# Optimization experiments

Measured on AMD Instinct MI355X. Metric: run time of the kernel, lower is better.

Reference implementation:

```python
import jax, jax.numpy as jnp
import numpy as np

K = 3          # kernel size
STRIDE = 1
PAD = 1
DIL = 1
K2 = K * K     # number of sampling locations per output pixel


def conv2d(x, w, b, stride=STRIDE, pad=PAD, dil=DIL):
    # x: [B,C,H,W], w: [O,I,K,K], b: [O]
    out = jax.lax.conv_general_dilated(
        x, w, window_strides=(stride, stride),
        padding=[(pad, pad), (pad, pad)], rhs_dilation=(dil, dil),
        dimension_numbers=('NCHW', 'OIHW', 'NCHW'))
    return out + b[None, :, None, None]


def bilinear_sample(x, sy, sx):
    # x: [B,C,H,W]; sy, sx: [B,K2,Ho,Wo] float sampling coords (y, x)
    # zero padding outside the image (torchvision deform_conv2d semantics)
    B, C, H, W = x.shape
    x_flat = x.reshape(B, C, H * W)

    y0 = jnp.floor(sy)
    x0 = jnp.floor(sx)
    wy1 = sy - y0  # frac weights
    wx1 = sx - x0
    wy0 = 1.0 - wy1
    wx0 = 1.0 - wx1

    def gather(yi, xi):
        valid = ((yi >= 0) & (yi < H) & (xi >= 0) & (xi < W)).astype(x.dtype)
        yc = jnp.clip(yi, 0, H - 1).astype(jnp.int32)
        xc = jnp.clip(xi, 0, W - 1).astype(jnp.int32)
        idx = (yc * W + xc).reshape(B, 1, -1)  # [B,1,K2*Ho*Wo]
        v = jnp.take_along_axis(x_flat, idx, axis=2)  # [B,C,K2*Ho*Wo]
        v = v.reshape(B, C, *yi.shape[1:])            # [B,C,K2,Ho,Wo]
        return v * valid[:, None]

    out = (gather(y0,     x0    ) * (wy0 * wx0)[:, None]
         + gather(y0,     x0 + 1) * (wy0 * wx1)[:, None]
         + gather(y0 + 1, x0    ) * (wy1 * wx0)[:, None]
         + gather(y0 + 1, x0 + 1) * (wy1 * wx1)[:, None])
    return out  # [B,C,K2,Ho,Wo]


def setup_inputs() -> dict:
    key = jax.random.key(0)
    ks = jax.random.split(key, 6)
    B, C, H, W = 4, 64, 128, 128
    Cout = 64
    x = jax.random.normal(ks[0], (B, C, H, W), jnp.float32)
    # offset conv: 2*K2 output channels; small init -> small offsets (realistic)
    w_off = jax.random.normal(ks[1], (2 * K2, C, K, K), jnp.float32) * 0.01
    b_off = jnp.zeros((2 * K2,), jnp.float32)
    # mask conv: K2 output channels, sigmoid activation
    w_mask = jax.random.normal(ks[2], (K2, C, K, K), jnp.float32) * 0.01
    b_mask = jnp.zeros((K2,), jnp.float32)  # mask_init_bias = 0
    # main deformable conv weights
    w = jax.random.normal(ks[3], (Cout, C, K, K), jnp.float32) * (1.0 / np.sqrt(C * K2))
    b = jnp.zeros((Cout,), jnp.float32)
    return {"x": x, "w_off": w_off, "b_off": b_off,
            "w_mask": w_mask, "b_mask": b_mask, "w": w, "b": b}


def reference(x, w_off, b_off, w_mask, b_mask, w, b):
    B, C, H, W = x.shape
    Cout = w.shape[0]

    offset = conv2d(x, w_off, b_off)                    # [B,2*K2,Ho,Wo]
    mask = jax.nn.sigmoid(conv2d(x, w_mask, b_mask))    # [B,K2,Ho,Wo]
    Ho, Wo = offset.shape[2], offset.shape[3]

    off = offset.reshape(B, K2, 2, Ho, Wo)
    dy, dx = off[:, :, 0], off[:, :, 1]                 # torchvision layout: (y,x) pairs

    ki = (jnp.arange(K2) // K).astype(jnp.float32)      # kernel row index
    kj = (jnp.arange(K2) % K).astype(jnp.float32)       # kernel col index
    base_y = (jnp.arange(Ho, dtype=jnp.float32) * STRIDE - PAD)[None, :, None] \
             + (ki * DIL)[:, None, None]                # [K2,Ho,1]
    base_x = (jnp.arange(Wo, dtype=jnp.float32) * STRIDE - PAD)[None, None, :] \
             + (kj * DIL)[:, None, None]                # [K2,1,Wo]

    sy = base_y[None] + dy                              # [B,K2,Ho,Wo]
    sx = base_x[None] + dx

    sampled = bilinear_sample(x, sy, sx) * mask[:, None]  # [B,C,K2,Ho,Wo]
    out = jnp.einsum('bckhw,ock->bohw', sampled, w.reshape(Cout, C, K2))
    return out + b[None, :, None, None]
```

## Files before the change

kernel.cpp:

```cpp
#include <hip/hip_runtime.h>
#include <math.h>

typedef __attribute__((ext_vector_type(8))) short short8;
typedef __attribute__((ext_vector_type(4))) float f32x4;
typedef unsigned short ushort_t;
typedef unsigned int uint_t;

#define HH 128
#define WW 128
#define CC 64
#define HWp 16384

__device__ inline ushort_t f2bf(float f) {
    uint_t u = __float_as_uint(f);
    uint_t r = (u + 0x7FFFu + ((u >> 16) & 1u)) >> 16;
    return (ushort_t)r;
}
__device__ inline float blo(uint_t u) { return __uint_as_float(u << 16); }
__device__ inline float bhi(uint_t u) { return __uint_as_float(u & 0xFFFF0000u); }
__device__ inline short8 bc8(uint4 v) { return __builtin_bit_cast(short8, v); }

__device__ inline uint_t pk2(f32x4 wv, uint_t a, uint_t b, uint_t c, uint_t d) {
    float lo = wv.x * blo(a) + wv.y * blo(b) + wv.z * blo(c) + wv.w * blo(d);
    float hi = wv.x * bhi(a) + wv.y * bhi(b) + wv.z * bhi(c) + wv.w * bhi(d);
    uint_t r;
    asm("v_cvt_pk_bf16_f32 %0, %1, %2" : "=v"(r) : "v"(lo), "v"(hi));
    return r;
}
__device__ inline short8 bilerp8(f32x4 wv, uint4 A, uint4 B, uint4 C, uint4 D) {
    uint4 r;
    r.x = pk2(wv, A.x, B.x, C.x, D.x);
    r.y = pk2(wv, A.y, B.y, C.y, D.y);
    r.z = pk2(wv, A.z, B.z, C.z, D.z);
    r.w = pk2(wv, A.w, B.w, C.w, D.w);
    return __builtin_bit_cast(short8, r);
}

__global__ __launch_bounds__(256) void k_prep(const float* __restrict__ x,
        ushort_t* __restrict__ xtb,
        const float* __restrict__ w_off, const float* __restrict__ w_mask,
        const float* __restrict__ w,
        ushort_t* __restrict__ wpom, ushort_t* __restrict__ wpm) {
    __shared__ __align__(16) float tile[64][68];
    int bid = blockIdx.x;
    int t = threadIdx.x;
    if (bid < 1024) {
        int xs = (bid & 1) * 64;
        int y  = (bid >> 1) & 127;
        int b  = bid >> 8;
#pragma unroll
        for (int i = 0; i < 4; ++i) {
            int c  = i * 16 + (t >> 4);
            int xl = (t & 15) << 2;
            float4 v = *(const float4*)&x[(((size_t)b * CC + c) * HH + y) * WW + xs + xl];
            *(float4*)&tile[c][xl] = v;
        }
        __syncthreads();
#pragma unroll
        for (int i = 0; i < 8; ++i) {
            int pxl = i * 8 + (t >> 5);
            int cp  = t & 31;
            float v0 = tile[cp * 2][pxl], v1 = tile[cp * 2 + 1][pxl];
            uint_t pk;
            asm("v_cvt_pk_bf16_f32 %0, %1, %2" : "=v"(pk) : "v"(v0), "v"(v1));
            *(uint_t*)&xtb[(((size_t)b * HH + y) * WW + xs + pxl) * CC + cp * 2] = pk;
        }
    } else {
        int idx = (bid - 1024) * 256 + t;
        if (idx < 18432) {
            int e = idx;
            int j = e & 7, l = (e >> 3) & 63, mf = (e >> 9) & 1, ks = e >> 10;
            int ch = mf * 16 + (l & 15);
            int k = ks * 32 + ((l >> 4) << 3) + j;
            int c = k & 63, kk = k >> 6;
            float v = 0.f;
            if (ch < 18) v = w_off[(ch * CC + c) * 9 + kk];
            else if (ch < 27) v = w_mask[((ch - 18) * CC + c) * 9 + kk];
            wpom[idx] = f2bf(v);
        } else if (idx < 18432 + 36864) {
            int e = idx - 18432;
            int j = e & 7, l = (e >> 3) & 63, mf = (e >> 9) & 3, ks = e >> 11;
            int o = mf * 16 + (l & 15);
            int k = ks * 32 + ((l >> 4) << 3) + j;
            int c = k & 63, kk = k >> 6;
            wpm[e] = f2bf(w[(o * CC + c) * 9 + kk]);
        }
    }
}

__global__ __launch_bounds__(256, 8) void k_conv_om(const ushort_t* __restrict__ xtb,
        const uint4* __restrict__ wpom, const float* __restrict__ b_off,
        const float* __restrict__ b_mask, float* __restrict__ om) {
    __shared__ ushort_t xrow[3 * 34 * 64];
    int blk = blockIdx.x;
    int b = blk >> 9, rem = blk & 511;
    int y = rem >> 2, xw = rem & 3;
    int xbase = (xw << 5) - 1;
    int t = threadIdx.x;

#pragma unroll
    for (int i = 0; i < 4; ++i) {
        int t2 = i * 256 + t;
        if (t2 < 816) {
            int ky = t2 / 272;
            int r2 = t2 - ky * 272;
            int cl = r2 >> 3, cj = r2 & 7;
            int yy = y + ky - 1;
            int xc = xbase + cl;
            bool ok = (yy >= 0) && (yy < HH) && (xc >= 0) && (xc < WW);
            uint4 v = make_uint4(0u, 0u, 0u, 0u);
            if (ok) v = *(const uint4*)&xtb[((size_t)b * HWp + yy * WW + xc) * CC + cj * 8];
            int idx = ((ky * 34 + cl) * 64 + cj * 8) ^ ((cl & 7) << 3);
            *(uint4*)&xrow[idx] = v;
        }
    }
    __syncthreads();

    int lane = t & 63, w = t >> 6;
    int mfc = w & 1, nfc = w >> 1;
    int lm = lane & 15, lg = lane >> 4;
    int pxl = (nfc << 4) + lm;
    f32x4 acc = {};
#pragma unroll
    for (int ks = 0; ks < 18; ++ks) {
        int kk = ks >> 1;
        int kyy = kk / 3, kxx = kk % 3;
        int c0 = (ks & 1) * 32 + lg * 8;
        short8 af = bc8(wpom[(ks * 2 + mfc) * 64 + lane]);
        int cl = pxl + kxx;
        int idx = ((kyy * 34 + cl) * 64 + c0) ^ ((cl & 7) << 3);
        short8 bf = *(const short8*)&xrow[idx];
        acc = __builtin_amdgcn_mfma_f32_16x16x32_bf16(af, bf, acc, 0, 0, 0);
    }
    int xg = (xw << 1) + nfc;
    size_t tb = ((size_t)((b * 128 + y) * 8 + xg)) * 432;
#pragma unroll
    for (int r = 0; r < 4; ++r) {
        int ch = (mfc << 4) + (lg << 2) + r;
        if (ch < 27) {
            float v = acc[r] + (ch < 18 ? b_off[ch] : b_mask[ch - 18]);
            if (ch >= 18) v = 1.f / (1.f + __expf(-v));
            om[tb + ch * 16 + lm] = v;
        }
    }
}

__global__ __launch_bounds__(256, 8) void k_fused(const ushort_t* __restrict__ xtb,
        const float* __restrict__ omt, const uint4* __restrict__ wpm,
        const float* __restrict__ bias, float* __restrict__ out) {
    __shared__ __align__(16) ushort_t sm[16 * 576];
    int blk = blockIdx.x;
    int b = blk >> 10, rem = blk & 1023;
    int y = rem >> 3, xg = rem & 7, xs = xg << 4;
    int t = threadIdx.x, lane = t & 63, w = t >> 6;
    const char* xbB = (const char*)xtb + ((size_t)b << 21);
    const float* omb = omt + ((size_t)((b * 128 + y) * 8 + xg)) * 432;

    float pw0 = 0.f, pw1 = 0.f, pw2 = 0.f, pw3 = 0.f;
    int paT = 0, paB = 0, ppk = 0;
    if (lane < 36) {
        int pxl = lane / 9, k = lane - pxl * 9;
        int px_t = (w << 2) + pxl;
        int ki = k / 3, kj = k - ki * 3;
        int x = xs + px_t;
        float dy = omb[32 * k + px_t];
        float dx = omb[32 * k + 16 + px_t];
        float m  = omb[288 + 16 * k + px_t];
        float sy = (float)(y - 1 + ki) + dy;
        float sx = (float)(x - 1 + kj) + dx;
        float fy = floorf(sy), fx = floorf(sx);
        float wy1 = sy - fy, wx1 = sx - fx;
        float wy0 = 1.f - wy1, wx0 = 1.f - wx1;
        int iy0 = (int)fy, ix0 = (int)fx;
        int iy1 = iy0 + 1, ix1 = ix0 + 1;
        bool vy0 = (iy0 >= 0) & (iy0 < HH);
        bool vy1 = (iy1 >= 0) & (iy1 < HH);
        float wyr0 = vy0 ? wy0 : (vy1 ? wy1 : 0.f);
        int   ry0  = vy0 ? iy0 : (vy1 ? iy1 : 0);
        float wyr1 = (vy0 & vy1) ? wy1 : 0.f;
        int   ry1  = min(max(iy1, 0), HH - 1);
        int bx = min(max(ix0, 0), WW - 2);
        float wxh0 = (bx == ix0) ? wx0 : ((bx == ix1) ? wx1 : 0.f);
        float wxh1 = (bx + 1 == ix1) ? wx1 : ((bx + 1 == ix0) ? wx0 : 0.f);
        pw0 = m * wyr0 * wxh0;
        pw1 = m * wyr0 * wxh1;
        pw2 = m * wyr1 * wxh0;
        pw3 = m * wyr1 * wxh1;
        paT = (int)((uint_t)(((ry0 << 7) + bx) << 7));
        paB = (int)((uint_t)(((ry1 << 7) + bx) << 7));
        ppk = (int)((uint_t)(px_t * 576 + k * 64) |
                    ((uint_t)(((px_t ^ k) & 7) << 3) << 16));
    }

    {
        int g = lane >> 3, j = lane & 7;
        uint_t j16 = (uint_t)(j << 4);
        uint_t jw  = (uint_t)(j << 3);
        int slA = g;
        float wA0 = __shfl(pw0, slA), wA1 = __shfl(pw1, slA);
        float wA2 = __shfl(pw2, slA), wA3 = __shfl(pw3, slA);
        uint_t aTA = (uint_t)__shfl(paT, slA) + j16;
        uint_t aBA = (uint_t)__shfl(paB, slA) + j16;
        uint_t pkA = (uint_t)__shfl(ppk, slA);
        uint4 tlA = *(const uint4*)(xbB + aTA);
        uint4 trA = *(const uint4*)(xbB + aTA + 128);
        uint4 blA = *(const uint4*)(xbB + aBA);
        uint4 brA = *(const uint4*)(xbB + aBA + 128);
#pragma unroll
        for (int r = 0; r < 5; ++r) {
            float wB0, wB1, wB2, wB3;
            uint_t pkB = 0;
            uint4 tlB, trB, blB, brB;
            if (r < 4) {
                int slB = g + (r + 1) * 8; slB = slB > 35 ? 35 : slB;
                wB0 = __shfl(pw0, slB); wB1 = __shfl(pw1, slB);
                wB2 = __shfl(pw2, slB); wB3 = __shfl(pw3, slB);
                uint_t aTB = (uint_t)__shfl(paT, slB) + j16;
                uint_t aBB = (uint_t)__shfl(paB, slB) + j16;
                pkB = (uint_t)__shfl(ppk, slB);
                tlB = *(const uint4*)(xbB + aTB);
                trB = *(const uint4*)(xbB + aTB + 128);
                blB = *(const uint4*)(xbB + aBB);
                brB = *(const uint4*)(xbB + aBB + 128);
            }
            f32x4 wv = { wA0, wA1, wA2, wA3 };
            short8 bf = bilerp8(wv, tlA, trA, blA, brA);
            if (r < 4 || g < 4) {
                uint_t widx = ((pkA & 0xFFFFu) + jw) ^ (pkA >> 16);
                *(short8*)&sm[widx] = bf;
            }
            wA0 = wB0; wA1 = wB1; wA2 = wB2; wA3 = wB3;
            pkA = pkB;
            tlA = tlB; trA = trB; blA = blB; brA = brB;
        }
    }
    __syncthreads();

    int lm = lane & 15, lg = lane >> 4;
    f32x4 acc = {};
#pragma unroll
    for (int ks = 0; ks < 18; ++ks) {
        short8 af = bc8(wpm[((ks << 2) + w) * 64 + lane]);
        int bidx = (lm * 576 + (ks << 5) + (lg << 3)) ^ (((lm ^ (ks >> 1)) & 7) << 3);
        short8 bf = *(const short8*)&sm[bidx];
        acc = __builtin_amdgcn_mfma_f32_16x16x32_bf16(af, bf, acc, 0, 0, 0);
    }
#pragma unroll
    for (int r = 0; r < 4; ++r) {
        int o = (w << 4) + (lg << 2) + r;
        out[(((size_t)b * 64 + o) << 14) + (y << 7) + xs + lm] = acc[r] + bias[o];
    }
}

extern "C" void kernel_launch(void* const* d_in, const int* in_sizes, int n_in,
                              void* d_out, int out_size, void* d_ws, size_t ws_size,
                              hipStream_t stream) {
    const float* x      = (const float*)d_in[0];
    const float* w_off  = (const float*)d_in[1];
    const float* b_off  = (const float*)d_in[2];
    const float* w_mask = (const float*)d_in[3];
    const float* b_mask = (const float*)d_in[4];
    const float* w      = (const float*)d_in[5];
    const float* bias   = (const float*)d_in[6];
    float* out = (float*)d_out;

    char* ws = (char*)d_ws;
    ushort_t* xtb  = (ushort_t*)(ws);
    float*    om   = (float*)(ws + 8388608);
    ushort_t* wpom = (ushort_t*)(ws + 15466496);
    ushort_t* wpm  = (ushort_t*)(ws + 15503360);

    hipLaunchKernelGGL(k_prep, dim3(1240), dim3(256), 0, stream,
                       x, xtb, w_off, w_mask, w, wpom, wpm);
    hipLaunchKernelGGL(k_conv_om, dim3(2048), dim3(256), 0, stream,
                       xtb, (const uint4*)wpom, b_off, b_mask, om);
    hipLaunchKernelGGL(k_fused, dim3(4096), dim3(256), 0, stream,
                       xtb, om, (const uint4*)wpm, bias, out);
}
```

Measured before the change: 48.58 us.

## Precompute bilinear sampling params in offset conv kernel, stream them to fused kernel

The offset/mask conv kernel now stages its outputs in shared memory and computes per-(pixel, tap) bilinear weights, clamped corner addresses and LDS store indices. It writes these as 32-byte records to global memory. The fused kernel loads the precomputed records directly instead of recomputing coordinates and broadcasting them with shuffles, and its occupancy hint drops from 8 to 7. The intermediate buffer grows from 27 floats per pixel to 72 floats per pixel, which increases global write and read traffic between the two kernels.

```diff
diff --git a/kernel.cpp b/kernel.cpp
--- a/kernel.cpp
+++ b/kernel.cpp
@@ -90,8 +90,9 @@
 
 __global__ __launch_bounds__(256, 8) void k_conv_om(const ushort_t* __restrict__ xtb,
         const uint4* __restrict__ wpom, const float* __restrict__ b_off,
-        const float* __restrict__ b_mask, float* __restrict__ om) {
+        const float* __restrict__ b_mask, float* __restrict__ prm) {
     __shared__ ushort_t xrow[3 * 34 * 64];
+    __shared__ float om_t[32][28];
     int blk = blockIdx.x;
     int b = blk >> 9, rem = blk & 511;
     int y = rem >> 2, xw = rem & 3;
@@ -116,37 +117,80 @@
     }
     __syncthreads();
 
-    int lane = t & 63, w = t >> 6;
-    int mfc = w & 1, nfc = w >> 1;
-    int lm = lane & 15, lg = lane >> 4;
-    int pxl = (nfc << 4) + lm;
-    f32x4 acc = {};
-#pragma unroll
-    for (int ks = 0; ks < 18; ++ks) {
-        int kk = ks >> 1;
-        int kyy = kk / 3, kxx = kk % 3;
-        int c0 = (ks & 1) * 32 + lg * 8;
-        short8 af = bc8(wpom[(ks * 2 + mfc) * 64 + lane]);
-        int cl = pxl + kxx;
-        int idx = ((kyy * 34 + cl) * 64 + c0) ^ ((cl & 7) << 3);
-        short8 bf = *(const short8*)&xrow[idx];
-        acc = __builtin_amdgcn_mfma_f32_16x16x32_bf16(af, bf, acc, 0, 0, 0);
-    }
-    int xg = (xw << 1) + nfc;
-    size_t tb = ((size_t)((b * 128 + y) * 8 + xg)) * 432;
-#pragma unroll
-    for (int r = 0; r < 4; ++r) {
-        int ch = (mfc << 4) + (lg << 2) + r;
-        if (ch < 27) {
-            float v = acc[r] + (ch < 18 ? b_off[ch] : b_mask[ch - 18]);
-            if (ch >= 18) v = 1.f / (1.f + __expf(-v));
-            om[tb + ch * 16 + lm] = v;
-        }
-    }
-}
-
-__global__ __launch_bounds__(256, 8) void k_fused(const ushort_t* __restrict__ xtb,
-        const float* __restrict__ omt, const uint4* __restrict__ wpm,
+    {
+        int lane = t & 63, w = t >> 6;
+        int mfc = w & 1, nfc = w >> 1;
+        int lm = lane & 15, lg = lane >> 4;
+        int pxl = (nfc << 4) + lm;
+        f32x4 acc = {};
+#pragma unroll
+        for (int ks = 0; ks < 18; ++ks) {
+            int kk = ks >> 1;
+            int kyy = kk / 3, kxx = kk % 3;
+            int c0 = (ks & 1) * 32 + lg * 8;
+            short8 af = bc8(wpom[(ks * 2 + mfc) * 64 + lane]);
+            int cl = pxl + kxx;
+            int idx = ((kyy * 34 + cl) * 64 + c0) ^ ((cl & 7) << 3);
+            short8 bf = *(const short8*)&xrow[idx];
+            acc = __builtin_amdgcn_mfma_f32_16x16x32_bf16(af, bf, acc, 0, 0, 0);
+        }
+#pragma unroll
+        for (int r = 0; r < 4; ++r) {
+            int ch = (mfc << 4) + (lg << 2) + r;
+            if (ch < 27) {
+                float v = acc[r] + (ch < 18 ? b_off[ch] : b_mask[ch - 18]);
+                if (ch >= 18) v = 1.f / (1.f + __expf(-v));
+                om_t[pxl][ch] = v;
+            }
+        }
+    }
+    __syncthreads();
+
+    size_t tbase = ((size_t)((b * 128 + y) * 8 + (xw << 1))) * 1152;
+#pragma unroll
+    for (int rep = 0; rep < 2; ++rep) {
+        int S = rep * 256 + t;
+        if (S < 288) {
+            int px32 = S / 9, k = S - px32 * 9;
+            int ki = k / 3, kj = k - ki * 3;
+            int x = (xw << 5) + px32;
+            int px_t = px32 & 15;
+            float dy = om_t[px32][2 * k];
+            float dx = om_t[px32][2 * k + 1];
+            float m  = om_t[px32][18 + k];
+            float sy = (float)(y - 1 + ki) + dy;
+            float sx = (float)(x - 1 + kj) + dx;
+            float fy = floorf(sy), fx = floorf(sx);
+            float wy1 = sy - fy, wx1 = sx - fx;
+            float wy0 = 1.f - wy1, wx0 = 1.f - wx1;
+            int iy0 = (int)fy, ix0 = (int)fx;
+            int iy1 = iy0 + 1, ix1 = ix0 + 1;
+            bool vy0 = (iy0 >= 0) & (iy0 < HH);
+            bool vy1 = (iy1 >= 0) & (iy1 < HH);
+            float wyr0 = vy0 ? wy0 : (vy1 ? wy1 : 0.f);
+            int   ry0  = vy0 ? iy0 : (vy1 ? iy1 : 0);
+            float wyr1 = (vy0 & vy1) ? wy1 : 0.f;
+            int   ry1  = min(max(iy1, 0), HH - 1);
+            int bx = min(max(ix0, 0), WW - 2);
+            float wxh0 = (bx == ix0) ? wx0 : ((bx == ix1) ? wx1 : 0.f);
+            float wxh1 = (bx + 1 == ix1) ? wx1 : ((bx + 1 == ix0) ? wx0 : 0.f);
+            f32x4 wv = { m * wyr0 * wxh0, m * wyr0 * wxh1,
+                         m * wyr1 * wxh0, m * wyr1 * wxh1 };
+            f32x4 aux;
+            aux.x = __uint_as_float((uint_t)(((ry0 << 7) + bx) << 7));
+            aux.y = __uint_as_float((uint_t)(((ry1 << 7) + bx) << 7));
+            aux.z = __uint_as_float((uint_t)(px_t * 576 + k * 64) |
+                                    ((uint_t)(((px_t ^ k) & 7) << 3) << 16));
+            aux.w = 0.f;
+            float* pp = prm + tbase + (size_t)S * 8;
+            *(f32x4*)pp = wv;
+            *(f32x4*)(pp + 4) = aux;
+        }
+    }
+}
+
+__global__ __launch_bounds__(256, 7) void k_fused(const ushort_t* __restrict__ xtb,
+        const float* __restrict__ prm, const uint4* __restrict__ wpm,
         const float* __restrict__ bias, float* __restrict__ out) {
     __shared__ __align__(16) ushort_t sm[16 * 576];
     int blk = blockIdx.x;
@@ -154,83 +198,41 @@
     int y = rem >> 3, xg = rem & 7, xs = xg << 4;
     int t = threadIdx.x, lane = t & 63, w = t >> 6;
     const char* xbB = (const char*)xtb + ((size_t)b << 21);
-    const float* omb = omt + ((size_t)((b * 128 + y) * 8 + xg)) * 432;
-
-    float pw0 = 0.f, pw1 = 0.f, pw2 = 0.f, pw3 = 0.f;
-    int paT = 0, paB = 0, ppk = 0;
-    if (lane < 36) {
-        int pxl = lane / 9, k = lane - pxl * 9;
-        int px_t = (w << 2) + pxl;
-        int ki = k / 3, kj = k - ki * 3;
-        int x = xs + px_t;
-        float dy = omb[32 * k + px_t];
-        float dx = omb[32 * k + 16 + px_t];
-        float m  = omb[288 + 16 * k + px_t];
-        float sy = (float)(y - 1 + ki) + dy;
-        float sx = (float)(x - 1 + kj) + dx;
-        float fy = floorf(sy), fx = floorf(sx);
-        float wy1 = sy - fy, wx1 = sx - fx;
-        float wy0 = 1.f - wy1, wx0 = 1.f - wx1;
-        int iy0 = (int)fy, ix0 = (int)fx;
-        int iy1 = iy0 + 1, ix1 = ix0 + 1;
-        bool vy0 = (iy0 >= 0) & (iy0 < HH);
-        bool vy1 = (iy1 >= 0) & (iy1 < HH);
-        float wyr0 = vy0 ? wy0 : (vy1 ? wy1 : 0.f);
-        int   ry0  = vy0 ? iy0 : (vy1 ? iy1 : 0);
-        float wyr1 = (vy0 & vy1) ? wy1 : 0.f;
-        int   ry1  = min(max(iy1, 0), HH - 1);
-        int bx = min(max(ix0, 0), WW - 2);
-        float wxh0 = (bx == ix0) ? wx0 : ((bx == ix1) ? wx1 : 0.f);
-        float wxh1 = (bx + 1 == ix1) ? wx1 : ((bx + 1 == ix0) ? wx0 : 0.f);
-        pw0 = m * wyr0 * wxh0;
-        pw1 = m * wyr0 * wxh1;
-        pw2 = m * wyr1 * wxh0;
-        pw3 = m * wyr1 * wxh1;
-        paT = (int)((uint_t)(((ry0 << 7) + bx) << 7));
-        paB = (int)((uint_t)(((ry1 << 7) + bx) << 7));
-        ppk = (int)((uint_t)(px_t * 576 + k * 64) |
-                    ((uint_t)(((px_t ^ k) & 7) << 3) << 16));
-    }
+    const float* pb = prm + ((size_t)((b * 128 + y) * 8 + xg)) * 1152 + w * (36 * 8);
 
     {
         int g = lane >> 3, j = lane & 7;
         uint_t j16 = (uint_t)(j << 4);
         uint_t jw  = (uint_t)(j << 3);
-        int slA = g;
-        float wA0 = __shfl(pw0, slA), wA1 = __shfl(pw1, slA);
-        float wA2 = __shfl(pw2, slA), wA3 = __shfl(pw3, slA);
-        uint_t aTA = (uint_t)__shfl(paT, slA) + j16;
-        uint_t aBA = (uint_t)__shfl(paB, slA) + j16;
-        uint_t pkA = (uint_t)__shfl(ppk, slA);
+        uint4 axv[5];
+        f32x4 wvv[5];
+#pragma unroll
+        for (int r = 0; r < 5; ++r) {
+            int sl = g + r * 8; sl = sl > 35 ? 35 : sl;
+            axv[r] = *(const uint4*)(pb + sl * 8 + 4);
+            wvv[r] = *(const f32x4*)(pb + sl * 8);
+        }
+        uint_t aTA = axv[0].x + j16, aBA = axv[0].y + j16;
         uint4 tlA = *(const uint4*)(xbB + aTA);
         uint4 trA = *(const uint4*)(xbB + aTA + 128);
         uint4 blA = *(const uint4*)(xbB + aBA);
         uint4 brA = *(const uint4*)(xbB + aBA + 128);
 #pragma unroll
         for (int r = 0; r < 5; ++r) {
-            float wB0, wB1, wB2, wB3;
-            uint_t pkB = 0;
             uint4 tlB, trB, blB, brB;
             if (r < 4) {
-                int slB = g + (r + 1) * 8; slB = slB > 35 ? 35 : slB;
-                wB0 = __shfl(pw0, slB); wB1 = __shfl(pw1, slB);
-                wB2 = __shfl(pw2, slB); wB3 = __shfl(pw3, slB);
-                uint_t aTB = (uint_t)__shfl(paT, slB) + j16;
-                uint_t aBB = (uint_t)__shfl(paB, slB) + j16;
-                pkB = (uint_t)__shfl(ppk, slB);
+                uint_t aTB = axv[r + 1].x + j16, aBB = axv[r + 1].y + j16;
                 tlB = *(const uint4*)(xbB + aTB);
                 trB = *(const uint4*)(xbB + aTB + 128);
                 blB = *(const uint4*)(xbB + aBB);
                 brB = *(const uint4*)(xbB + aBB + 128);
             }
-            f32x4 wv = { wA0, wA1, wA2, wA3 };
-            short8 bf = bilerp8(wv, tlA, trA, blA, brA);
+            short8 bf = bilerp8(wvv[r], tlA, trA, blA, brA);
             if (r < 4 || g < 4) {
+                uint_t pkA = axv[r].z;
                 uint_t widx = ((pkA & 0xFFFFu) + jw) ^ (pkA >> 16);
                 *(short8*)&sm[widx] = bf;
             }
-            wA0 = wB0; wA1 = wB1; wA2 = wB2; wA3 = wB3;
-            pkA = pkB;
             tlA = tlB; trA = trB; blA = blB; brA = brB;
         }
     }
@@ -266,14 +268,14 @@
 
     char* ws = (char*)d_ws;
     ushort_t* xtb  = (ushort_t*)(ws);
-    float*    om   = (float*)(ws + 8388608);
-    ushort_t* wpom = (ushort_t*)(ws + 15466496);
-    ushort_t* wpm  = (ushort_t*)(ws + 15503360);
+    float*    prm  = (float*)(ws + 8388608);
+    ushort_t* wpom = (ushort_t*)(ws + 27262976);
+    ushort_t* wpm  = (ushort_t*)(ws + 27299840);
 
     hipLaunchKernelGGL(k_prep, dim3(1240), dim3(256), 0, stream,
                        x, xtb, w_off, w_mask, w, wpom, wpm);
     hipLaunchKernelGGL(k_conv_om, dim3(2048), dim3(256), 0, stream,
-                       xtb, (const uint4*)wpom, b_off, b_mask, om);
+                       xtb, (const uint4*)wpom, b_off, b_mask, prm);
     hipLaunchKernelGGL(k_fused, dim3(4096), dim3(256), 0, stream,
-                       xtb, om, (const uint4*)wpm, bias, out);
-}
+                       xtb, prm, (const uint4*)wpm, bias, out);
+}
```

Measured after the change: 53.47 us. +10.1%, slower.

## Fuse NCHW-to-NHWC bf16 transpose into offset/mask conv kernel

Applied to the files above, without the earlier changes.

Removes the transpose stage from the prep kernel. The offset/mask conv kernel now reads fp32 NCHW input directly, converts it to bf16 into shared memory, and writes its centre row out to the NHWC bf16 buffer used by the fused kernel. This drops one full read-write pass over the activations and makes the weight-pack kernel tiny. The cost is that each conv block reads its three input rows as scalar fp32 loads with 3x row redundancy instead of vectorised bf16 loads.

```diff
diff --git a/kernel.cpp b/kernel.cpp
--- a/kernel.cpp
+++ b/kernel.cpp
@@ -36,85 +36,90 @@
     return __builtin_bit_cast(short8, r);
 }
 
-__global__ __launch_bounds__(256) void k_prep(const float* __restrict__ x,
-        ushort_t* __restrict__ xtb,
-        const float* __restrict__ w_off, const float* __restrict__ w_mask,
-        const float* __restrict__ w,
+__global__ __launch_bounds__(256) void k_pack(const float* __restrict__ w_off,
+        const float* __restrict__ w_mask, const float* __restrict__ w,
         ushort_t* __restrict__ wpom, ushort_t* __restrict__ wpm) {
-    __shared__ __align__(16) float tile[64][68];
-    int bid = blockIdx.x;
-    int t = threadIdx.x;
-    if (bid < 1024) {
-        int xs = (bid & 1) * 64;
-        int y  = (bid >> 1) & 127;
-        int b  = bid >> 8;
-#pragma unroll
-        for (int i = 0; i < 4; ++i) {
-            int c  = i * 16 + (t >> 4);
-            int xl = (t & 15) << 2;
-            float4 v = *(const float4*)&x[(((size_t)b * CC + c) * HH + y) * WW + xs + xl];
-            *(float4*)&tile[c][xl] = v;
-        }
-        __syncthreads();
-#pragma unroll
-        for (int i = 0; i < 8; ++i) {
-            int pxl = i * 8 + (t >> 5);
-            int cp  = t & 31;
-            float v0 = tile[cp * 2][pxl], v1 = tile[cp * 2 + 1][pxl];
-            uint_t pk;
-            asm("v_cvt_pk_bf16_f32 %0, %1, %2" : "=v"(pk) : "v"(v0), "v"(v1));
-            *(uint_t*)&xtb[(((size_t)b * HH + y) * WW + xs + pxl) * CC + cp * 2] = pk;
-        }
-    } else {
-        int idx = (bid - 1024) * 256 + t;
-        if (idx < 18432) {
-            int e = idx;
-            int j = e & 7, l = (e >> 3) & 63, mf = (e >> 9) & 1, ks = e >> 10;
-            int ch = mf * 16 + (l & 15);
-            int k = ks * 32 + ((l >> 4) << 3) + j;
-            int c = k & 63, kk = k >> 6;
-            float v = 0.f;
-            if (ch < 18) v = w_off[(ch * CC + c) * 9 + kk];
-            else if (ch < 27) v = w_mask[((ch - 18) * CC + c) * 9 + kk];
-            wpom[idx] = f2bf(v);
-        } else if (idx < 18432 + 36864) {
-            int e = idx - 18432;
-            int j = e & 7, l = (e >> 3) & 63, mf = (e >> 9) & 3, ks = e >> 11;
-            int o = mf * 16 + (l & 15);
-            int k = ks * 32 + ((l >> 4) << 3) + j;
-            int c = k & 63, kk = k >> 6;
-            wpm[e] = f2bf(w[(o * CC + c) * 9 + kk]);
-        }
-    }
-}
-
-__global__ __launch_bounds__(256, 8) void k_conv_om(const ushort_t* __restrict__ xtb,
-        const uint4* __restrict__ wpom, const float* __restrict__ b_off,
-        const float* __restrict__ b_mask, float* __restrict__ om) {
+    int idx = blockIdx.x * 256 + threadIdx.x;
+    if (idx < 18432) {
+        int e = idx;
+        int j = e & 7, l = (e >> 3) & 63, mf = (e >> 9) & 1, ks = e >> 10;
+        int ch = mf * 16 + (l & 15);
+        int k = ks * 32 + ((l >> 4) << 3) + j;
+        int c = k & 63, kk = k >> 6;
+        float v = 0.f;
+        if (ch < 18) v = w_off[(ch * CC + c) * 9 + kk];
+        else if (ch < 27) v = w_mask[((ch - 18) * CC + c) * 9 + kk];
+        wpom[idx] = f2bf(v);
+    } else if (idx < 18432 + 36864) {
+        int e = idx - 18432;
+        int j = e & 7, l = (e >> 3) & 63, mf = (e >> 9) & 3, ks = e >> 11;
+        int o = mf * 16 + (l & 15);
+        int k = ks * 32 + ((l >> 4) << 3) + j;
+        int c = k & 63, kk = k >> 6;
+        wpm[e] = f2bf(w[(o * CC + c) * 9 + kk]);
+    }
+}
+
+__global__ __launch_bounds__(256, 8) void k_conv_om(const float* __restrict__ x,
+        ushort_t* __restrict__ xtb, const uint4* __restrict__ wpom,
+        const float* __restrict__ b_off, const float* __restrict__ b_mask,
+        float* __restrict__ om) {
     __shared__ ushort_t xrow[3 * 34 * 64];
     int blk = blockIdx.x;
     int b = blk >> 9, rem = blk & 511;
     int y = rem >> 2, xw = rem & 3;
-    int xbase = (xw << 5) - 1;
     int t = threadIdx.x;
 
-#pragma unroll
-    for (int i = 0; i < 4; ++i) {
-        int t2 = i * 256 + t;
-        if (t2 < 816) {
-            int ky = t2 / 272;
-            int r2 = t2 - ky * 272;
-            int cl = r2 >> 3, cj = r2 & 7;
+    {
+        int px = t & 31;
+        int grp = t >> 5;
+        int xc = (xw << 5) + px;
+#pragma unroll
+        for (int it = 0; it < 12; ++it) {
+            int slot = it * 8 + grp;
+            int ky = slot >> 5;
+            int cpair = slot & 31;
             int yy = y + ky - 1;
-            int xc = xbase + cl;
-            bool ok = (yy >= 0) && (yy < HH) && (xc >= 0) && (xc < WW);
-            uint4 v = make_uint4(0u, 0u, 0u, 0u);
-            if (ok) v = *(const uint4*)&xtb[((size_t)b * HWp + yy * WW + xc) * CC + cj * 8];
-            int idx = ((ky * 34 + cl) * 64 + cj * 8) ^ ((cl & 7) << 3);
-            *(uint4*)&xrow[idx] = v;
-        }
+            float v0 = 0.f, v1 = 0.f;
+            if (yy >= 0 && yy < HH) {
+                size_t base = ((size_t)(b * CC + 2 * cpair) * HH + yy) * WW + xc;
+                v0 = x[base];
+                v1 = x[base + (size_t)HWp];
+            }
+            uint_t pk;
+            asm("v_cvt_pk_bf16_f32 %0, %1, %2" : "=v"(pk) : "v"(v0), "v"(v1));
+            int cl = px + 1;
+            int idx = ((ky * 34 + cl) * 64 + 2 * cpair) ^ ((cl & 7) << 3);
+            *(uint_t*)&xrow[idx] = pk;
+        }
+    }
+    if (t < 192) {
+        int ky = t >> 6, r = t & 63, cpair = r >> 1, side = r & 1;
+        int yy = y + ky - 1;
+        int xc = side ? (xw << 5) + 32 : (xw << 5) - 1;
+        bool ok = (yy >= 0) && (yy < HH) && (xc >= 0) && (xc < WW);
+        float v0 = 0.f, v1 = 0.f;
+        if (ok) {
+            size_t base = ((size_t)(b * CC + 2 * cpair) * HH + yy) * WW + xc;
+            v0 = x[base];
+            v1 = x[base + (size_t)HWp];
+        }
+        uint_t pk;
+        asm("v_cvt_pk_bf16_f32 %0, %1, %2" : "=v"(pk) : "v"(v0), "v"(v1));
+        int cl = side ? 33 : 0;
+        int idx = ((ky * 34 + cl) * 64 + 2 * cpair) ^ ((cl & 7) << 3);
+        *(uint_t*)&xrow[idx] = pk;
     }
     __syncthreads();
+
+    {
+        int px2 = t >> 3;
+        int cj = t & 7;
+        int cl = px2 + 1;
+        int idx = ((34 + cl) * 64 + cj * 8) ^ ((cl & 7) << 3);
+        uint4 v = *(const uint4*)&xrow[idx];
+        *(uint4*)&xtb[((size_t)b * HWp + y * WW + (xw << 5) + px2) * CC + cj * 8] = v;
+    }
 
     int lane = t & 63, w = t >> 6;
     int mfc = w & 1, nfc = w >> 1;
@@ -270,10 +275,10 @@
     ushort_t* wpom = (ushort_t*)(ws + 15466496);
     ushort_t* wpm  = (ushort_t*)(ws + 15503360);
 
-    hipLaunchKernelGGL(k_prep, dim3(1240), dim3(256), 0, stream,
-                       x, xtb, w_off, w_mask, w, wpom, wpm);
+    hipLaunchKernelGGL(k_pack, dim3(216), dim3(256), 0, stream,
+                       w_off, w_mask, w, wpom, wpm);
     hipLaunchKernelGGL(k_conv_om, dim3(2048), dim3(256), 0, stream,
-                       xtb, (const uint4*)wpom, b_off, b_mask, om);
+                       x, xtb, (const uint4*)wpom, b_off, b_mask, om);
     hipLaunchKernelGGL(k_fused, dim3(4096), dim3(256), 0, stream,
                        xtb, om, (const uint4*)wpm, bias, out);
 }
```

Result: slower. 54.88 us (+13.0%).
